# Kernel tuning notes

Hardware: AMD Instinct MI355X
Metric: run time of the kernel (lower is better)

Reference implementation:

```python
import jax, jax.numpy as jnp
from jax import lax
import numpy as np

K = 3          # k_size
STRIDE = 1
LAMDA = 10.0
B, H, W_, D = 2, 64, 64, 64


def extract_patches(x, k, stride, same):
    """TF tf.image.extract_patches layout: per-position vector ordered (ki, kj, channel)."""
    b, h, w, d = x.shape
    kn = (k - 1) // 2
    if same:  # SAME padding, stride 1 (as used for fg patches)
        x = jnp.pad(x, ((0, 0), (kn, kn), (kn, kn), (0, 0)))
        ph, pw = h, w
    else:     # VALID with stride
        ph = (h - k) // stride + 1
        pw = (w - k) // stride + 1
    cols = [x[:, i:i + (ph - 1) * stride + 1:stride, j:j + (pw - 1) * stride + 1:stride, :]
            for i in range(k) for j in range(k)]
    return jnp.stack(cols, axis=3).reshape(b, ph, pw, k * k * d)


def setup_inputs() -> dict:
    key = jax.random.key(0)
    k1, k2, k3, k4 = jax.random.split(key, 4)
    bg_in = jax.random.normal(k1, (B, H, W_, D), jnp.float32)
    fg_in = jax.random.normal(k2, (B, H, W_, D), jnp.float32)
    m = (jax.random.uniform(k3, (B, H, W_, 1)) > 0.3).astype(jnp.float32)
    mask = jnp.broadcast_to(m, (B, H, W_, D)) + jnp.zeros((), jnp.float32)
    W_ml = jax.random.normal(k4, (2 * D, D), jnp.float32) * 0.05  # 1x1 conv 'ML'
    b_ml = jnp.zeros((D,), jnp.float32)
    return {"bg_in": bg_in, "fg_in": fg_in, "mask": mask, "W_ml": W_ml, "b_ml": b_ml}


def reference(bg_in, fg_in, mask, W_ml, b_ml):
    b, h, w, d = bg_in.shape
    kn = (K - 1) // 2
    # nearest resize to (h,w) is identity here; take channel 0, tile to d channels
    mask_r = jnp.broadcast_to(mask[..., :1], (b, h, w, d))
    bg = bg_in * mask_r
    ph = (h - K) // STRIDE + 1
    pw = (w - K) // STRIDE + 1
    c = ph * pw
    # background patches: (b, c, k*k*d); foreground patches: (b, h, w, k*k*d)
    patch1 = extract_patches(bg, K, STRIDE, False).reshape(b, c, K * K * d)
    patch2 = extract_patches(fg_in, K, 1, True)
    k1d = jnp.sum(patch1 * patch1, axis=2)          # (b, c)
    wwd = jnp.sum(patch2 * patch2, axis=3)          # (b, h, w)
    # 1x1 conv of fg patches against bg patch bank == cross-correlation
    CS = jnp.einsum('bhwp,bcp->bhwc', patch2, patch1)
    DS1 = k1d[:, None, None, :] + wwd[..., None] - 2.0 * CS   # squared distances (b,h,w,c)
    mu = jnp.mean(DS1, axis=-1, keepdims=True)
    sd = jnp.std(DS1, axis=-1, keepdims=True)       # population std, as tf.math.reduce_std
    DS2 = -jnp.tanh((DS1 - mu) / sd)
    # exp(x-3)/sum(exp(x-3)) == softmax(x)
    CA = jax.nn.softmax(LAMDA * DS2, axis=-1)       # (b, h, w, c)
    # per-sample transposed conv with bg patches as kernel (k2: (b,K,K,d,c))
    k2 = patch1.reshape(b, c, K, K, d).transpose(0, 2, 3, 4, 1)
    # tf.nn.conv2d_transpose == gradient of SAME conv: correlate with rot180 kernel, swap I/O
    kt = k2[:, ::-1, ::-1].transpose(0, 1, 2, 4, 3)  # (b, K, K, c, d)

    def tconv(ca, ker):
        return lax.conv_general_dilated(ca[None], ker, (1, 1), 'SAME',
                                        dimension_numbers=('NHWC', 'HWIO', 'NHWC'))[0]

    ACL = jax.vmap(tconv)(CA, kt) / float(K * K)    # (b, h, w, d)
    ACL = bg + ACL * (1.0 - mask_r)
    con1 = jnp.concatenate([bg_in, ACL], axis=-1)   # (b, h, w, 2d)
    out = jax.nn.elu(jnp.einsum('bhwc,co->bhwo', con1, W_ml) + b_ml)
    return out
```

## Files before the change

kernel.cpp:

```cpp
#include <hip/hip_runtime.h>
#include <hip/hip_fp16.h>
#include <math.h>

#define BB 2
#define HH 64
#define WW 64
#define DD 64
#define PH 62
#define CC 3844
#define CCP 3968
#define PL 576
#define PLP 640
#define TP 8
#define LAM 10.0f

typedef _Float16 f16;
typedef __attribute__((ext_vector_type(8))) _Float16 half8;
typedef __attribute__((ext_vector_type(4))) float f32x4;

#define REQ_FAST 90030080ULL

__device__ __forceinline__ void gld16(const void* g, void* l) {
  __builtin_amdgcn_global_load_lds((const __attribute__((address_space(1))) void*)g,
                                   (__attribute__((address_space(3))) void*)l, 16, 0, 0);
}

__global__ __launch_bounds__(256) void k_prepA(
    const float* __restrict__ bg_in, const float* __restrict__ fg,
    const float* __restrict__ mask, f16* __restrict__ bgf,
    f16* __restrict__ fgp, float* __restrict__ s2) {
  const int NBG = BB * 4288 * 64;
  const int NFG = BB * 4356 * 64;
  int idx = blockIdx.x * 256 + threadIdx.x;
  if (idx < NBG) {
    int ch = idx & 63;
    int pix = (idx >> 6) % 4288;
    int b = idx / (4288 * 64);
    f16 v = (f16)0.f;
    if (pix < 4096) {
      size_t src = ((size_t)b * 4096 + pix) * 64 + ch;
      v = (f16)(bg_in[src] * mask[((size_t)b * 4096 + pix) * 64]);
    }
    bgf[idx] = v;
  } else if (idx < NBG + NFG) {
    int i2 = idx - NBG;
    int ch = i2 & 63;
    int pix = (i2 >> 6) % 4356;
    int b = i2 / (4356 * 64);
    int yy = pix / 66, xx = pix - 66 * yy;
    float v = 0.f;
    if (yy >= 1 && yy <= 64 && xx >= 1 && xx <= 64)
      v = fg[(((size_t)b * 64 + (yy - 1)) * 64 + (xx - 1)) * 64 + ch];
    fgp[i2] = (f16)v;
  } else {
    int i3 = idx - (NBG + NFG);
    int q = i3 & 15;
    int pix = (i3 >> 4) & 4095;
    int b = i3 >> 16;
    float4 v = ((const float4*)(bg_in + ((size_t)b * 4096 + pix) * 64))[q];
    float a = v.x * v.x + v.y * v.y + v.z * v.z + v.w * v.w;
    a += __shfl_xor(a, 1, 64);
    a += __shfl_xor(a, 2, 64);
    a += __shfl_xor(a, 4, 64);
    a += __shfl_xor(a, 8, 64);
    if (q == 0) {
      float m = mask[((size_t)b * 4096 + pix) * 64];
      s2[b * 4096 + pix] = m * m * a;
    }
  }
}

__global__ __launch_bounds__(256) void k_prepB(
    const f16* __restrict__ bgf, const float* __restrict__ s2,
    f16* __restrict__ P1T, float* __restrict__ k1d) {
  __shared__ f16 st[62 * 66];
  const int NB1 = 31;
  if (blockIdx.x < NB1) {
    int idx = blockIdx.x * 256 + threadIdx.x;
    if (idx < BB * CC) {
      int b = idx / CC, c = idx - b * CC;
      int ci = c / PH, cj = c - ci * PH;
      float s = 0.f;
#pragma unroll
      for (int ki = 0; ki < 3; ++ki)
#pragma unroll
        for (int kj = 0; kj < 3; ++kj)
          s += s2[b * 4096 + (ci + ki) * 64 + cj + kj];
      k1d[(size_t)b * CCP + c] = s;
    }
    return;
  }
  int pb = blockIdx.x - NB1;
  int ci = pb % 63;
  int rest = pb / 63;
  int kk = rest % 9;
  int b = rest / 9;
  int ki = kk / 3, kj = kk - 3 * ki;
  f16* P1Tb = P1T + (size_t)b * PLP * CCP;
  if (ci == 62) {
    for (int i = threadIdx.x; i < 64 * 124; i += 256) {
      int ch = i / 124, cc = i - ch * 124;
      P1Tb[(size_t)(kk * 64 + ch) * CCP + CC + cc] = (f16)0.f;
    }
    return;
  }
  const f16* src = bgf + (size_t)b * (4288 * 64) + (size_t)((ci + ki) * 64 + kj) * 64;
  for (int i = threadIdx.x; i < 496; i += 256) {
    half8 v = ((const half8*)src)[i];
    int p = i >> 3, ch0 = (i & 7) * 8;
#pragma unroll
    for (int j = 0; j < 8; ++j) st[p * 66 + ch0 + j] = v[j];
  }
  __syncthreads();
  for (int i = threadIdx.x; i < 64 * 62; i += 256) {
    int ch = i / 62, cj = i - ch * 62;
    P1Tb[(size_t)(kk * 64 + ch) * CCP + ci * 62 + cj] = st[cj * 66 + ch];
  }
}

__global__ __launch_bounds__(512) void k_gemm1(
    const f16* __restrict__ fgp, const f16* __restrict__ bgf,
    f16* __restrict__ CS) {
  __shared__ f16 tA[2][128 * 64];
  __shared__ f16 tB[2][128 * 64];
  const int tid = threadIdx.x;
  const int l = tid & 63, w = tid >> 6;
  const int b = blockIdx.z;
  const int m0 = blockIdx.y * 128, n0 = blockIdx.x * 128;
  const f16* fgB = fgp + (size_t)b * (4356 * 64);
  const f16* bgB = bgf + (size_t)b * (4288 * 64);

  int pixA[2], chSA[2], aCh[2];
#pragma unroll
  for (int i = 0; i < 2; ++i) {
    aCh[i] = w * 2 + i;
    int li = aCh[i] * 64 + l;
    int r = li >> 3;
    int j = (li & 7) ^ (r & 7);
    chSA[i] = j * 8;
    int pos = m0 + r;
    pixA[i] = (pos >> 6) * 66 + (pos & 63);
  }
  int pixB[2], chSB[2], bCh[2];
#pragma unroll
  for (int i = 0; i < 2; ++i) {
    bCh[i] = w * 2 + i;
    int li = bCh[i] * 64 + l;
    int r = li >> 3;
    int j = (li & 7) ^ (r & 7);
    chSB[i] = j * 8;
    int c = n0 + r;
    if (c < CC) {
      int ci = c / 62;
      pixB[i] = ci * 64 + (c - 62 * ci);
    } else {
      pixB[i] = 4096;
    }
  }

  const int wm = (w >> 2) * 64, wn = (w & 3) * 32;
  const int lr = l & 15, lk = l >> 4;
  const int xr = (lr & 7) << 4;

  f32x4 acc[4][2];
#pragma unroll
  for (int mi = 0; mi < 4; ++mi)
#pragma unroll
    for (int ni = 0; ni < 2; ++ni) acc[mi][ni] = (f32x4){0.f, 0.f, 0.f, 0.f};

#pragma unroll
  for (int i = 0; i < 2; ++i) {
    gld16(fgB + (size_t)pixA[i] * 64 + chSA[i], (char*)tA[0] + aCh[i] * 1024);
    gld16(bgB + (size_t)pixB[i] * 64 + chSB[i], (char*)tB[0] + bCh[i] * 1024);
  }
  asm volatile("s_waitcnt vmcnt(0)" ::: "memory");
  __syncthreads();

#pragma unroll 1
  for (int t = 0; t < 9; ++t) {
    const int cur = t & 1;
    if (t + 1 < 9) {
      const int tn = t + 1;
      const int ki = tn / 3, kj = tn - 3 * ki;
      const int offA = ki * 66 + kj, offB = ki * 64 + kj;
#pragma unroll
      for (int i = 0; i < 2; ++i) {
        gld16(fgB + (size_t)(pixA[i] + offA) * 64 + chSA[i],
              (char*)tA[cur ^ 1] + aCh[i] * 1024);
        gld16(bgB + (size_t)(pixB[i] + offB) * 64 + chSB[i],
              (char*)tB[cur ^ 1] + bCh[i] * 1024);
      }
    }
#pragma unroll
    for (int kk = 0; kk < 2; ++kk) {
      half8 av[4], bv[2];
      const int cb = lk * 16 + kk * 64;
#pragma unroll
      for (int mi = 0; mi < 4; ++mi) {
        int r = wm + mi * 16 + lr;
        av[mi] = *(const half8*)((const char*)tA[cur] + r * 128 + (cb ^ xr));
      }
#pragma unroll
      for (int ni = 0; ni < 2; ++ni) {
        int r = wn + ni * 16 + lr;
        bv[ni] = *(const half8*)((const char*)tB[cur] + r * 128 + (cb ^ xr));
      }
#pragma unroll
      for (int mi = 0; mi < 4; ++mi)
#pragma unroll
        for (int ni = 0; ni < 2; ++ni)
          acc[mi][ni] = __builtin_amdgcn_mfma_f32_16x16x32_f16(
              av[mi], bv[ni], acc[mi][ni], 0, 0, 0);
    }
    asm volatile("s_waitcnt vmcnt(0)" ::: "memory");
    __syncthreads();
  }

  CS += (size_t)b * 4096 * CCP;
#pragma unroll
  for (int mi = 0; mi < 4; ++mi) {
#pragma unroll
    for (int q = 0; q < 4; ++q) {
      int m = m0 + wm + mi * 16 + lk * 4 + q;
#pragma unroll
      for (int ni = 0; ni < 2; ++ni) {
        int n = n0 + wn + ni * 16 + lr;
        CS[(size_t)m * CCP + n] = (f16)acc[mi][ni][q];
      }
    }
  }
}

__global__ __launch_bounds__(512) void k_gemm2(
    const f16* __restrict__ A, const f16* __restrict__ B, f16* __restrict__ C,
    const float* __restrict__ sden) {
  __shared__ f16 tA[2][64 * 64];
  __shared__ f16 tB[2][128 * 64];
  const int tid = threadIdx.x;
  const int l = tid & 63, w = tid >> 6;
  const int p = blockIdx.x;
  const int L = (p & 7) * 80 + (p >> 3);
  const int b = L / 320;
  const int rL = L - b * 320;
  const int mt = rL / 5, nt = rL - mt * 5;
  const int m0 = mt * 64, n0 = nt * 128;
  A += (size_t)b * 4096 * CCP;
  B += (size_t)b * PLP * CCP;
  C += (size_t)b * 4096 * PLP;
  const float* sd = sden + (size_t)b * 4096;

  size_t aOff;
  {
    int li = w * 64 + l;
    int r = li >> 3;
    int j = (li & 7) ^ (r & 7);
    aOff = (size_t)(m0 + r) * CCP + j * 8;
  }
  size_t bOff[2];
  int bCh[2];
#pragma unroll
  for (int i = 0; i < 2; ++i) {
    bCh[i] = w * 2 + i;
    int li = bCh[i] * 64 + l;
    int r = li >> 3;
    int j = (li & 7) ^ (r & 7);
    bOff[i] = (size_t)(n0 + r) * CCP + j * 8;
  }

  const int wm = (w >> 2) * 32, wn = (w & 3) * 32;
  const int lr = l & 15, lk = l >> 4;
  const int xr = (lr & 7) << 4;

  f32x4 acc[2][2];
#pragma unroll
  for (int mi = 0; mi < 2; ++mi)
#pragma unroll
    for (int ni = 0; ni < 2; ++ni) acc[mi][ni] = (f32x4){0.f, 0.f, 0.f, 0.f};

  auto STAGE = [&](int buf, int k0) {
    gld16(A + aOff + k0, (char*)tA[buf] + w * 1024);
#pragma unroll
    for (int i = 0; i < 2; ++i)
      gld16(B + bOff[i] + k0, (char*)tB[buf] + bCh[i] * 1024);
  };

  const int NT = CCP / 64;
  STAGE(0, 0);
  asm volatile("s_waitcnt vmcnt(0)" ::: "memory");
  __syncthreads();

#pragma unroll 1
  for (int t = 0; t < NT; ++t) {
    const int cur = t & 1;
    if (t + 1 < NT) STAGE(cur ^ 1, (t + 1) * 64);
#pragma unroll
    for (int kk = 0; kk < 2; ++kk) {
      half8 av[2], bv[2];
      const int cb = lk * 16 + kk * 64;
#pragma unroll
      for (int mi = 0; mi < 2; ++mi) {
        int r = wm + mi * 16 + lr;
        av[mi] = *(const half8*)((const char*)tA[cur] + r * 128 + (cb ^ xr));
      }
#pragma unroll
      for (int ni = 0; ni < 2; ++ni) {
        int r = wn + ni * 16 + lr;
        bv[ni] = *(const half8*)((const char*)tB[cur] + r * 128 + (cb ^ xr));
      }
#pragma unroll
      for (int mi = 0; mi < 2; ++mi)
#pragma unroll
        for (int ni = 0; ni < 2; ++ni)
          acc[mi][ni] = __builtin_amdgcn_mfma_f32_16x16x32_f16(
              av[mi], bv[ni], acc[mi][ni], 0, 0, 0);
    }
    asm volatile("s_waitcnt vmcnt(0)" ::: "memory");
    __syncthreads();
  }

#pragma unroll
  for (int mi = 0; mi < 2; ++mi) {
#pragma unroll
    for (int q = 0; q < 4; ++q) {
      int m = m0 + wm + mi * 16 + lk * 4 + q;
      float sc = sd[m];
#pragma unroll
      for (int ni = 0; ni < 2; ++ni) {
        int n = n0 + wn + ni * 16 + lr;
        C[(size_t)m * PLP + n] = (f16)(acc[mi][ni][q] * sc);
      }
    }
  }
}

__global__ __launch_bounds__(256) void k_stats(f16* __restrict__ CS,
                                               const float* __restrict__ k1d,
                                               float* __restrict__ sden) {
  __shared__ float red[8];
  const int tid = threadIdx.x;
  const int row = blockIdx.x, b = blockIdx.y;
  f16* cs = CS + ((size_t)b * 4096 + row) * CCP;
  const float* kd = k1d + (size_t)b * CCP;
  const int base = tid * 16;
  const bool act = base < CCP;

  float tv[16];
  float s1 = 0.f, s2 = 0.f;
  if (act) {
    half8 v0 = ((const half8*)(cs + base))[0];
    half8 v1 = ((const half8*)(cs + base))[1];
    float kv[16];
    *(float4*)(kv + 0) = ((const float4*)(kd + base))[0];
    *(float4*)(kv + 4) = ((const float4*)(kd + base))[1];
    *(float4*)(kv + 8) = ((const float4*)(kd + base))[2];
    *(float4*)(kv + 12) = ((const float4*)(kd + base))[3];
#pragma unroll
    for (int i = 0; i < 16; ++i) {
      float cval = (float)(i < 8 ? v0[i] : v1[i - 8]);
      float t = (base + i < CC) ? (kv[i] - 2.f * cval) : 0.f;
      tv[i] = t;
      s1 += t;
      s2 = fmaf(t, t, s2);
    }
  } else {
#pragma unroll
    for (int i = 0; i < 16; ++i) tv[i] = 0.f;
  }
#pragma unroll
  for (int m = 32; m; m >>= 1) {
    s1 += __shfl_xor(s1, m, 64);
    s2 += __shfl_xor(s2, m, 64);
  }
  if ((tid & 63) == 0) {
    red[tid >> 6] = s1;
    red[4 + (tid >> 6)] = s2;
  }
  __syncthreads();
  float mu = (red[0] + red[1] + red[2] + red[3]) * (1.f / CC);
  float ex2 = (red[4] + red[5] + red[6] + red[7]) * (1.f / CC);
  float var = fmaxf(ex2 - mu * mu, 1e-12f);
  float rsd = rsqrtf(var);
  __syncthreads();

  float den = 0.f;
  if (act) {
    half8 w0, w1;
#pragma unroll
    for (int i = 0; i < 16; ++i) {
      float wv = 0.f;
      if (base + i < CC) {
        float z = (tv[i] - mu) * rsd;
        float e2z = __expf(2.f * z);
        float th = 1.f - 2.f / (e2z + 1.f);
        wv = __expf(-LAM * th);
        den += wv;
      }
      if (i < 8) w0[i] = (f16)wv; else w1[i - 8] = (f16)wv;
    }
    ((half8*)(cs + base))[0] = w0;
    ((half8*)(cs + base))[1] = w1;
  }
#pragma unroll
  for (int m = 32; m; m >>= 1) den += __shfl_xor(den, m, 64);
  if ((tid & 63) == 0) red[tid >> 6] = den;
  __syncthreads();
  if (tid == 0)
    sden[(size_t)b * 4096 + row] = 1.f / (9.f * (red[0] + red[1] + red[2] + red[3]));
}

__global__ __launch_bounds__(256) void k_final2(
    const float* __restrict__ bg_in, const float* __restrict__ mask,
    const f16* __restrict__ N2, const float* __restrict__ Wml,
    const float* __restrict__ bml, float* __restrict__ out) {
  __shared__ float s_con[4 * 128];
  const int tid = threadIdx.x;
  const int posg = blockIdx.x * 4;
  for (int i = tid; i < 4 * 128; i += 256) {
    int p = i >> 7, c = i & 127;
    int pos = posg + p;
    float v;
    if (c < 64) {
      v = bg_in[(size_t)pos * DD + c];
    } else {
      int cc = c - 64;
      int bwx = pos & 4095, bb = pos >> 12;
      int y = bwx >> 6, x = bwx & 63;
      float a = 0.f;
#pragma unroll
      for (int s = 0; s < 3; ++s) {
        int yy = y + 1 - s;
        if (yy < 0 || yy >= HH) continue;
#pragma unroll
        for (int t = 0; t < 3; ++t) {
          int xx = x + 1 - t;
          if (xx < 0 || xx >= WW) continue;
          a += (float)N2[((size_t)bb * 4096 + yy * 64 + xx) * PLP + (s * 3 + t) * 64 + cc];
        }
      }
      float m0 = mask[(size_t)pos * DD];
      v = bg_in[(size_t)pos * DD + cc] * m0 + a * (1.f - m0);
    }
    s_con[i] = v;
  }
  __syncthreads();
  const int o = tid & 63, p = tid >> 6;
  float sum = bml[o];
  const float* cp = s_con + (p << 7);
#pragma unroll 8
  for (int c = 0; c < 128; ++c) sum = fmaf(cp[c], Wml[c * 64 + o], sum);
  out[(size_t)(posg + p) * 64 + o] = (sum > 0.f) ? sum : expm1f(sum);
}

#define WS_BG    0
#define WS_BGT   524288
#define WS_K1D   1048576
#define WS_ACLN  1056264

__global__ __launch_bounds__(256) void k_prep(
    const float* __restrict__ bg_in, const float* __restrict__ mask,
    float* __restrict__ bg, float* __restrict__ bgT) {
  int idx = blockIdx.x * 256 + threadIdx.x;
  if (idx >= BB * HH * WW * DD) return;
  int ch = idx & 63, pos = idx >> 6;
  float m = mask[(size_t)pos * DD];
  float v = bg_in[idx] * m;
  bg[idx] = v;
  int x = pos & 63, rest = pos >> 6;
  int y = rest & 63, b = rest >> 6;
  bgT[(((size_t)b * DD + ch) * HH + y) * WW + x] = v;
}

__global__ __launch_bounds__(256) void k_k1d(const float* __restrict__ bg,
                                             float* __restrict__ k1d) {
  int idx = blockIdx.x * 256 + threadIdx.x;
  if (idx >= BB * CC) return;
  int b = idx / CC, c = idx - b * CC;
  int ci = c / PH, cj = c - ci * PH;
  float s = 0.f;
  for (int ki = 0; ki < 3; ++ki)
    for (int kj = 0; kj < 3; ++kj) {
      const float4* p =
          (const float4*)(bg + (((size_t)(b * HH + ci + ki) * WW) + cj + kj) * DD);
#pragma unroll
      for (int q = 0; q < 16; ++q) {
        float4 v = p[q];
        s += v.x * v.x + v.y * v.y + v.z * v.z + v.w * v.w;
      }
    }
  k1d[idx] = s;
}

__global__ __launch_bounds__(256, 2) void k_heavy(
    const float* __restrict__ fg, const float* __restrict__ bg,
    const float* __restrict__ bgT, const float* __restrict__ k1d,
    float* __restrict__ acln) {
  __shared__ _Float16 s_cs[TP * CC];
  __shared__ float s_fg[TP * PL];
  __shared__ float s_red[8];
  __shared__ float s_wwd[TP];
  __shared__ float s_den[TP];

  const int tid = threadIdx.x;
  const int X0 = blockIdx.x * TP;
  const int Y = blockIdx.y;
  const int b = blockIdx.z;

  for (int i = tid; i < TP * PL; i += 256) {
    int p = i / PL, r = i - p * PL;
    int kk = r >> 6, ch = r & 63;
    int ki = kk / 3, kj = kk - 3 * ki;
    int hy = Y + ki - 1, wx = X0 + p + kj - 1;
    float v = 0.f;
    if (hy >= 0 && hy < HH && wx >= 0 && wx < WW)
      v = fg[(((size_t)b * HH + hy) * WW + wx) * DD + ch];
    s_fg[i] = v;
  }
  __syncthreads();
  {
    int p = tid >> 5, lane = tid & 31;
    float a = 0.f;
    for (int r = lane; r < PL; r += 32) {
      float v = s_fg[p * PL + r];
      a = fmaf(v, v, a);
    }
#pragma unroll
    for (int m = 16; m; m >>= 1) a += __shfl_xor(a, m, 64);
    if (lane == 0) s_wwd[p] = a;
  }
  __syncthreads();

  const float* bgTb = bgT + (size_t)b * DD * HH * WW;
  for (int sw = 0; sw < 4; ++sw) {
    const int cb = sw * 256 + tid;
    float acc[TP][4];
#pragma unroll
    for (int p = 0; p < TP; ++p)
#pragma unroll
      for (int q = 0; q < 4; ++q) acc[p][q] = 0.f;
    int off4[4];
#pragma unroll
    for (int q = 0; q < 4; ++q) {
      int c = cb + q * 1024;
      if (c >= CC) c = CC - 1;
      int ci = c / PH;
      off4[q] = ci * WW + (c - ci * PH);
    }
    for (int ch = 0; ch < DD; ++ch) {
      const float* bgTc = bgTb + (size_t)ch * (HH * WW);
#pragma unroll
      for (int kk = 0; kk < 9; ++kk) {
        const int ki = kk / 3, kj = kk - 3 * (kk / 3);
        float fv[TP];
#pragma unroll
        for (int p = 0; p < TP; ++p) fv[p] = s_fg[p * PL + (kk << 6) + ch];
        float bv[4];
#pragma unroll
        for (int q = 0; q < 4; ++q) bv[q] = bgTc[off4[q] + ki * WW + kj];
#pragma unroll
        for (int p = 0; p < TP; ++p)
#pragma unroll
          for (int q = 0; q < 4; ++q) acc[p][q] = fmaf(fv[p], bv[q], acc[p][q]);
      }
    }
#pragma unroll
    for (int q = 0; q < 4; ++q) {
      int c = cb + q * 1024;
      if (c < CC) {
#pragma unroll
        for (int p = 0; p < TP; ++p) s_cs[p * CC + c] = (_Float16)acc[p][q];
      }
    }
  }
  __syncthreads();

  const float* k1db = k1d + b * CC;
  for (int pos = 0; pos < TP; ++pos) {
    __syncthreads();
    const float wwdp = s_wwd[pos];
    float s1 = 0.f, s2 = 0.f;
    for (int c = tid; c < CC; c += 256) {
      float ds1 = k1db[c] + wwdp - 2.f * (float)s_cs[pos * CC + c];
      s1 += ds1;
      s2 = fmaf(ds1, ds1, s2);
    }
#pragma unroll
    for (int m = 32; m; m >>= 1) {
      s1 += __shfl_xor(s1, m, 64);
      s2 += __shfl_xor(s2, m, 64);
    }
    if ((tid & 63) == 0) {
      int w = tid >> 6;
      s_red[w] = s1;
      s_red[4 + w] = s2;
    }
    __syncthreads();
    float mu = (s_red[0] + s_red[1] + s_red[2] + s_red[3]) * (1.f / CC);
    float ex2 = (s_red[4] + s_red[5] + s_red[6] + s_red[7]) * (1.f / CC);
    float var = fmaxf(ex2 - mu * mu, 1e-12f);
    float rsd = rsqrtf(var);
    float dp = 0.f;
    for (int c = tid; c < CC; c += 256) {
      float ds1 = k1db[c] + wwdp - 2.f * (float)s_cs[pos * CC + c];
      float z = (ds1 - mu) * rsd;
      float wv = expf(-LAM * tanhf(z));
      s_cs[pos * CC + c] = (_Float16)wv;
      dp += wv;
    }
#pragma unroll
    for (int m = 32; m; m >>= 1) dp += __shfl_xor(dp, m, 64);
    __syncthreads();
    if ((tid & 63) == 0) s_red[tid >> 6] = dp;
    __syncthreads();
    if (tid == 0) s_den[pos] = s_red[0] + s_red[1] + s_red[2] + s_red[3];
  }

  const int d = tid & 63;
  const int grp = tid >> 6;
  const int oA = grp, oB = grp + 4;
  const int sA = oA / 3, tA = oA - 3 * sA;
  const int sB = oB / 3, tB = oB - 3 * sB;
  const bool hasC = (grp == 0);
  const int offA = (sA * WW + tA) * DD + d;
  const int offB = (sB * WW + tB) * DD + d;
  const int offC = (2 * WW + 2) * DD + d;
  float aA[TP], aB[TP], aC[TP];
#pragma unroll
  for (int p = 0; p < TP; ++p) { aA[p] = 0.f; aB[p] = 0.f; aC[p] = 0.f; }
  const float* bgb = bg + (size_t)b * HH * WW * DD;
  float* s_wf = s_fg;
  int cj = 0, rowoff = 0;
  for (int c0 = 0; c0 < CC; c0 += 128) {
    const int n = (CC - c0 < 128) ? (CC - c0) : 128;
    __syncthreads();
    for (int i = tid; i < TP * 128; i += 256) {
      int p = i >> 7, cc = i & 127;
      s_wf[i] = (cc < n) ? (float)s_cs[p * CC + c0 + cc] : 0.f;
    }
    __syncthreads();
    for (int cc = 0; cc < n; cc += 2) {
      float2 wv[TP];
#pragma unroll
      for (int p = 0; p < TP; ++p)
        wv[p] = *(const float2*)(s_wf + (p << 7) + cc);
      {
        const float* rp = bgb + (size_t)rowoff * DD;
        float bA = rp[offA], bB = rp[offB], bCv = rp[offC];
#pragma unroll
        for (int p = 0; p < TP; ++p) {
          aA[p] = fmaf(wv[p].x, bA, aA[p]);
          aB[p] = fmaf(wv[p].x, bB, aB[p]);
          if (hasC) aC[p] = fmaf(wv[p].x, bCv, aC[p]);
        }
        ++rowoff;
        if (++cj == PH) { cj = 0; rowoff += 2; }
      }
      {
        const float* rp = bgb + (size_t)rowoff * DD;
        float bA = rp[offA], bB = rp[offB], bCv = rp[offC];
#pragma unroll
        for (int p = 0; p < TP; ++p) {
          aA[p] = fmaf(wv[p].y, bA, aA[p]);
          aB[p] = fmaf(wv[p].y, bB, aB[p]);
          if (hasC) aC[p] = fmaf(wv[p].y, bCv, aC[p]);
        }
        ++rowoff;
        if (++cj == PH) { cj = 0; rowoff += 2; }
      }
    }
  }
  __syncthreads();
#pragma unroll
  for (int p = 0; p < TP; ++p) {
    const float inv = 1.f / (9.f * s_den[p]);
    float* dst = acln + ((((size_t)b * HH + Y) * WW + (X0 + p)) * 9) * 64;
    dst[oA * 64 + d] = aA[p] * inv;
    dst[oB * 64 + d] = aB[p] * inv;
    if (hasC) dst[512 + d] = aC[p] * inv;
  }
}

__global__ __launch_bounds__(256) void k_final(
    const float* __restrict__ bg_in, const float* __restrict__ mask,
    const float* __restrict__ bg, const float* __restrict__ acln,
    const float* __restrict__ Wml, const float* __restrict__ bml,
    float* __restrict__ out) {
  __shared__ float s_con[4 * 128];
  const int tid = threadIdx.x;
  const int posg = blockIdx.x * 4;
  for (int i = tid; i < 4 * 128; i += 256) {
    int p = i >> 7, c = i & 127;
    int pos = posg + p;
    float v;
    if (c < 64) {
      v = bg_in[(size_t)pos * DD + c];
    } else {
      int cc = c - 64;
      int bwx = pos & 4095, bb = pos >> 12;
      int y = bwx >> 6, x = bwx & 63;
      float a = 0.f;
#pragma unroll
      for (int s = 0; s < 3; ++s) {
        int yy = y + 1 - s;
        if (yy < 0 || yy >= HH) continue;
#pragma unroll
        for (int t = 0; t < 3; ++t) {
          int xx = x + 1 - t;
          if (xx < 0 || xx >= WW) continue;
          a += acln[((((size_t)bb * HH + yy) * WW + xx) * 9 + (s * 3 + t)) * 64 + cc];
        }
      }
      float m0 = mask[(size_t)pos * DD];
      v = bg[(size_t)pos * DD + cc] + a * (1.f - m0);
    }
    s_con[i] = v;
  }
  __syncthreads();
  const int o = tid & 63, p = tid >> 6;
  float sum = bml[o];
  const float* cp = s_con + (p << 7);
#pragma unroll 8
  for (int c = 0; c < 128; ++c) sum = fmaf(cp[c], Wml[c * 64 + o], sum);
  out[(size_t)(posg + p) * 64 + o] = (sum > 0.f) ? sum : expm1f(sum);
}

extern "C" void kernel_launch(void* const* d_in, const int* in_sizes, int n_in,
                              void* d_out, int out_size, void* d_ws, size_t ws_size,
                              hipStream_t stream) {
  const float* bg_in = (const float*)d_in[0];
  const float* fg_in = (const float*)d_in[1];
  const float* mask = (const float*)d_in[2];
  const float* Wml = (const float*)d_in[3];
  const float* bml = (const float*)d_in[4];
  float* out = (float*)d_out;

  if (ws_size >= REQ_FAST) {
    char* w8 = (char*)d_ws;
    float* s2 = (float*)(w8 + 0);
    f16* fgp = (f16*)(w8 + 2097152);
    f16* bgf = (f16*)(w8 + 3212288);
    f16* P1T = (f16*)(w8 + 4310016);
    f16* CS = (f16*)(w8 + 14468096);
    f16* N2 = (f16*)(w8 + 79479808);
    float* k1d = (float*)(w8 + 89965568);
    float* sden = (float*)(w8 + 89997312);

    const int NA = BB * 4288 * 64 + BB * 4356 * 64 + BB * 4096 * 16;
    k_prepA<<<dim3((NA + 255) / 256), dim3(256), 0, stream>>>(
        bg_in, fg_in, mask, bgf, fgp, s2);
    k_prepB<<<dim3(31 + 63 * 9 * 2), dim3(256), 0, stream>>>(bgf, s2, P1T, k1d);
    k_gemm1<<<dim3(CCP / 128, 32, 2), dim3(512), 0, stream>>>(fgp, bgf, CS);
    k_stats<<<dim3(4096, 2), dim3(256), 0, stream>>>(CS, k1d, sden);
    k_gemm2<<<dim3(640), dim3(512), 0, stream>>>(CS, P1T, N2, sden);
    k_final2<<<dim3(2048), dim3(256), 0, stream>>>(bg_in, mask, N2, Wml, bml, out);
  } else {
    float* ws = (float*)d_ws;
    float* bg = ws + WS_BG;
    float* bgT = ws + WS_BGT;
    float* k1d = ws + WS_K1D;
    float* acln = ws + WS_ACLN;
    k_prep<<<dim3(2048), dim3(256), 0, stream>>>(bg_in, mask, bg, bgT);
    k_k1d<<<dim3((BB * CC + 255) / 256), dim3(256), 0, stream>>>(bg, k1d);
    k_heavy<<<dim3(8, 64, 2), dim3(256), 0, stream>>>(fg_in, bg, bgT, k1d, acln);
    k_final<<<dim3(2048), dim3(256), 0, stream>>>(bg_in, mask, bg, acln, Wml, bml, out);
  }
}
```

Measured before the change: 164.6 us.

## Recompute softmax weights inside gemm2 A-load instead of writing them in stats

k_stats no longer writes the exp/tanh weights back over the CS matrix. It only stores per-row mean, rstd and the normalizer. gemm2 loads the raw CS tile through registers, recomputes the weights on the fly and stores them into LDS, with the B tile still loaded by direct-to-LDS. This drops a full write pass over the large CS buffer. In exchange, the transcendental math is redone in every gemm2 block that shares a row (five column tiles), and the A path moves from async LDS loads to synchronous register loads.

```diff
diff --git a/kernel.cpp b/kernel.cpp
--- a/kernel.cpp
+++ b/kernel.cpp
@@ -231,9 +231,83 @@
   }
 }
 
+__global__ __launch_bounds__(256) void k_stats(const f16* __restrict__ CS,
+                                               const float* __restrict__ k1d,
+                                               float* __restrict__ rstat) {
+  __shared__ float red[8];
+  const int tid = threadIdx.x;
+  const int row = blockIdx.x, b = blockIdx.y;
+  const f16* cs = CS + ((size_t)b * 4096 + row) * CCP;
+  const float* kd = k1d + (size_t)b * CCP;
+  const int base = tid * 16;
+  const bool act = base < CCP;
+
+  float tv[16];
+  float s1 = 0.f, s2 = 0.f;
+  if (act) {
+    half8 v0 = ((const half8*)(cs + base))[0];
+    half8 v1 = ((const half8*)(cs + base))[1];
+    float kv[16];
+    *(float4*)(kv + 0) = ((const float4*)(kd + base))[0];
+    *(float4*)(kv + 4) = ((const float4*)(kd + base))[1];
+    *(float4*)(kv + 8) = ((const float4*)(kd + base))[2];
+    *(float4*)(kv + 12) = ((const float4*)(kd + base))[3];
+#pragma unroll
+    for (int i = 0; i < 16; ++i) {
+      float cval = (float)(i < 8 ? v0[i] : v1[i - 8]);
+      float t = (base + i < CC) ? (kv[i] - 2.f * cval) : 0.f;
+      tv[i] = t;
+      s1 += t;
+      s2 = fmaf(t, t, s2);
+    }
+  } else {
+#pragma unroll
+    for (int i = 0; i < 16; ++i) tv[i] = 0.f;
+  }
+#pragma unroll
+  for (int m = 32; m; m >>= 1) {
+    s1 += __shfl_xor(s1, m, 64);
+    s2 += __shfl_xor(s2, m, 64);
+  }
+  if ((tid & 63) == 0) {
+    red[tid >> 6] = s1;
+    red[4 + (tid >> 6)] = s2;
+  }
+  __syncthreads();
+  float mu = (red[0] + red[1] + red[2] + red[3]) * (1.f / CC);
+  float ex2 = (red[4] + red[5] + red[6] + red[7]) * (1.f / CC);
+  float var = fmaxf(ex2 - mu * mu, 1e-12f);
+  float rsd = rsqrtf(var);
+  __syncthreads();
+
+  float den = 0.f;
+  if (act) {
+#pragma unroll
+    for (int i = 0; i < 16; ++i) {
+      if (base + i < CC) {
+        float z = (tv[i] - mu) * rsd;
+        float e2z = __expf(2.f * z);
+        float th = 1.f - 2.f / (e2z + 1.f);
+        den += __expf(-LAM * th);
+      }
+    }
+  }
+#pragma unroll
+  for (int m = 32; m; m >>= 1) den += __shfl_xor(den, m, 64);
+  if ((tid & 63) == 0) red[tid >> 6] = den;
+  __syncthreads();
+  if (tid == 0) {
+    float dtot = red[0] + red[1] + red[2] + red[3];
+    float* o = rstat + ((size_t)b * 4096 + row) * 4;
+    o[0] = mu;
+    o[1] = rsd;
+    o[2] = 1.f / (9.f * dtot);
+  }
+}
+
 __global__ __launch_bounds__(512) void k_gemm2(
     const f16* __restrict__ A, const f16* __restrict__ B, f16* __restrict__ C,
-    const float* __restrict__ sden) {
+    const float* __restrict__ k1d, const float* __restrict__ rstat) {
   __shared__ f16 tA[2][64 * 64];
   __shared__ f16 tB[2][128 * 64];
   const int tid = threadIdx.x;
@@ -247,23 +321,25 @@
   A += (size_t)b * 4096 * CCP;
   B += (size_t)b * PLP * CCP;
   C += (size_t)b * 4096 * PLP;
-  const float* sd = sden + (size_t)b * 4096;
-
-  size_t aOff;
-  {
-    int li = w * 64 + l;
-    int r = li >> 3;
-    int j = (li & 7) ^ (r & 7);
-    aOff = (size_t)(m0 + r) * CCP + j * 8;
-  }
+  const float* kd = k1d + (size_t)b * CCP;
+  const float* rs = rstat + (size_t)b * 4096 * 4;
+
+  const int li = w * 64 + l;
+  const int aR = li >> 3;
+  const int aJ = (li & 7) ^ (aR & 7);
+  const size_t aOff = (size_t)(m0 + aR) * CCP + aJ * 8;
+  const int aCol0 = aJ * 8;
+  const float muR = rs[(m0 + aR) * 4 + 0];
+  const float rsdR = rs[(m0 + aR) * 4 + 1];
+
   size_t bOff[2];
   int bCh[2];
 #pragma unroll
   for (int i = 0; i < 2; ++i) {
     bCh[i] = w * 2 + i;
-    int li = bCh[i] * 64 + l;
-    int r = li >> 3;
-    int j = (li & 7) ^ (r & 7);
+    int li2 = bCh[i] * 64 + l;
+    int r = li2 >> 3;
+    int j = (li2 & 7) ^ (r & 7);
     bOff[i] = (size_t)(n0 + r) * CCP + j * 8;
   }
 
@@ -277,22 +353,49 @@
 #pragma unroll
     for (int ni = 0; ni < 2; ++ni) acc[mi][ni] = (f32x4){0.f, 0.f, 0.f, 0.f};
 
-  auto STAGE = [&](int buf, int k0) {
-    gld16(A + aOff + k0, (char*)tA[buf] + w * 1024);
-#pragma unroll
-    for (int i = 0; i < 2; ++i)
-      gld16(B + bOff[i] + k0, (char*)tB[buf] + bCh[i] * 1024);
+  auto XF = [&](half8 a8, float4 k0v, float4 k1v, int k0) -> half8 {
+    half8 w8;
+#pragma unroll
+    for (int e = 0; e < 8; ++e) {
+      float kv = (e < 4) ? ((e == 0) ? k0v.x : (e == 1) ? k0v.y : (e == 2) ? k0v.z : k0v.w)
+                         : ((e == 4) ? k1v.x : (e == 5) ? k1v.y : (e == 6) ? k1v.z : k1v.w);
+      float wv = 0.f;
+      if (aCol0 + k0 + e < CC) {
+        float t = kv - 2.f * (float)a8[e];
+        float z = (t - muR) * rsdR;
+        float e2z = __expf(2.f * z);
+        float th = 1.f - 2.f / (e2z + 1.f);
+        wv = __expf(-LAM * th);
+      }
+      w8[e] = (f16)wv;
+    }
+    return w8;
   };
 
   const int NT = CCP / 64;
-  STAGE(0, 0);
-  asm volatile("s_waitcnt vmcnt(0)" ::: "memory");
+  {
+    half8 a8 = *(const half8*)(A + aOff);
+    float4 k0v = *(const float4*)(kd + aCol0);
+    float4 k1v = *(const float4*)(kd + aCol0 + 4);
+    gld16(B + bOff[0], (char*)tB[0] + bCh[0] * 1024);
+    gld16(B + bOff[1], (char*)tB[0] + bCh[1] * 1024);
+    *(half8*)((char*)tA[0] + li * 16) = XF(a8, k0v, k1v, 0);
+  }
   __syncthreads();
 
 #pragma unroll 1
   for (int t = 0; t < NT; ++t) {
     const int cur = t & 1;
-    if (t + 1 < NT) STAGE(cur ^ 1, (t + 1) * 64);
+    half8 a8n;
+    float4 k0n, k1n;
+    if (t + 1 < NT) {
+      const int k0 = (t + 1) * 64;
+      a8n = *(const half8*)(A + aOff + k0);
+      k0n = *(const float4*)(kd + aCol0 + k0);
+      k1n = *(const float4*)(kd + aCol0 + k0 + 4);
+      gld16(B + bOff[0] + k0, (char*)tB[cur ^ 1] + bCh[0] * 1024);
+      gld16(B + bOff[1] + k0, (char*)tB[cur ^ 1] + bCh[1] * 1024);
+    }
 #pragma unroll
     for (int kk = 0; kk < 2; ++kk) {
       half8 av[2], bv[2];
@@ -314,7 +417,8 @@
           acc[mi][ni] = __builtin_amdgcn_mfma_f32_16x16x32_f16(
               av[mi], bv[ni], acc[mi][ni], 0, 0, 0);
     }
-    asm volatile("s_waitcnt vmcnt(0)" ::: "memory");
+    if (t + 1 < NT)
+      *(half8*)((char*)tA[cur ^ 1] + li * 16) = XF(a8n, k0n, k1n, (t + 1) * 64);
     __syncthreads();
   }
 
@@ -323,7 +427,7 @@
 #pragma unroll
     for (int q = 0; q < 4; ++q) {
       int m = m0 + wm + mi * 16 + lk * 4 + q;
-      float sc = sd[m];
+      float sc = rs[m * 4 + 2];
 #pragma unroll
       for (int ni = 0; ni < 2; ++ni) {
         int n = n0 + wn + ni * 16 + lr;
@@ -331,81 +435,6 @@
       }
     }
   }
-}
-
-__global__ __launch_bounds__(256) void k_stats(f16* __restrict__ CS,
-                                               const float* __restrict__ k1d,
-                                               float* __restrict__ sden) {
-  __shared__ float red[8];
-  const int tid = threadIdx.x;
-  const int row = blockIdx.x, b = blockIdx.y;
-  f16* cs = CS + ((size_t)b * 4096 + row) * CCP;
-  const float* kd = k1d + (size_t)b * CCP;
-  const int base = tid * 16;
-  const bool act = base < CCP;
-
-  float tv[16];
-  float s1 = 0.f, s2 = 0.f;
-  if (act) {
-    half8 v0 = ((const half8*)(cs + base))[0];
-    half8 v1 = ((const half8*)(cs + base))[1];
-    float kv[16];
-    *(float4*)(kv + 0) = ((const float4*)(kd + base))[0];
-    *(float4*)(kv + 4) = ((const float4*)(kd + base))[1];
-    *(float4*)(kv + 8) = ((const float4*)(kd + base))[2];
-    *(float4*)(kv + 12) = ((const float4*)(kd + base))[3];
-#pragma unroll
-    for (int i = 0; i < 16; ++i) {
-      float cval = (float)(i < 8 ? v0[i] : v1[i - 8]);
-      float t = (base + i < CC) ? (kv[i] - 2.f * cval) : 0.f;
-      tv[i] = t;
-      s1 += t;
-      s2 = fmaf(t, t, s2);
-    }
-  } else {
-#pragma unroll
-    for (int i = 0; i < 16; ++i) tv[i] = 0.f;
-  }
-#pragma unroll
-  for (int m = 32; m; m >>= 1) {
-    s1 += __shfl_xor(s1, m, 64);
-    s2 += __shfl_xor(s2, m, 64);
-  }
-  if ((tid & 63) == 0) {
-    red[tid >> 6] = s1;
-    red[4 + (tid >> 6)] = s2;
-  }
-  __syncthreads();
-  float mu = (red[0] + red[1] + red[2] + red[3]) * (1.f / CC);
-  float ex2 = (red[4] + red[5] + red[6] + red[7]) * (1.f / CC);
-  float var = fmaxf(ex2 - mu * mu, 1e-12f);
-  float rsd = rsqrtf(var);
-  __syncthreads();
-
-  float den = 0.f;
-  if (act) {
-    half8 w0, w1;
-#pragma unroll
-    for (int i = 0; i < 16; ++i) {
-      float wv = 0.f;
-      if (base + i < CC) {
-        float z = (tv[i] - mu) * rsd;
-        float e2z = __expf(2.f * z);
-        float th = 1.f - 2.f / (e2z + 1.f);
-        wv = __expf(-LAM * th);
-        den += wv;
-      }
-      if (i < 8) w0[i] = (f16)wv; else w1[i - 8] = (f16)wv;
-    }
-    ((half8*)(cs + base))[0] = w0;
-    ((half8*)(cs + base))[1] = w1;
-  }
-#pragma unroll
-  for (int m = 32; m; m >>= 1) den += __shfl_xor(den, m, 64);
-  if ((tid & 63) == 0) red[tid >> 6] = den;
-  __syncthreads();
-  if (tid == 0)
-    sden[(size_t)b * 4096 + row] = 1.f / (9.f * (red[0] + red[1] + red[2] + red[3]));
 }
 
 __global__ __launch_bounds__(256) void k_final2(
@@ -736,21 +765,21 @@
   if (ws_size >= REQ_FAST) {
     char* w8 = (char*)d_ws;
     float* s2 = (float*)(w8 + 0);
+    float* rstat = (float*)(w8 + 524288);
     f16* fgp = (f16*)(w8 + 2097152);
     f16* bgf = (f16*)(w8 + 3212288);
     f16* P1T = (f16*)(w8 + 4310016);
     f16* CS = (f16*)(w8 + 14468096);
     f16* N2 = (f16*)(w8 + 79479808);
     float* k1d = (float*)(w8 + 89965568);
-    float* sden = (float*)(w8 + 89997312);
 
     const int NA = BB * 4288 * 64 + BB * 4356 * 64 + BB * 4096 * 16;
     k_prepA<<<dim3((NA + 255) / 256), dim3(256), 0, stream>>>(
         bg_in, fg_in, mask, bgf, fgp, s2);
     k_prepB<<<dim3(31 + 63 * 9 * 2), dim3(256), 0, stream>>>(bgf, s2, P1T, k1d);
     k_gemm1<<<dim3(CCP / 128, 32, 2), dim3(512), 0, stream>>>(fgp, bgf, CS);
-    k_stats<<<dim3(4096, 2), dim3(256), 0, stream>>>(CS, k1d, sden);
-    k_gemm2<<<dim3(640), dim3(512), 0, stream>>>(CS, P1T, N2, sden);
+    k_stats<<<dim3(4096, 2), dim3(256), 0, stream>>>(CS, k1d, rstat);
+    k_gemm2<<<dim3(640), dim3(512), 0, stream>>>(CS, P1T, N2, k1d, rstat);
     k_final2<<<dim3(2048), dim3(256), 0, stream>>>(bg_in, mask, N2, Wml, bml, out);
   } else {
     float* ws = (float*)d_ws;
```

Result: slower. 274.9 us (+67.0%).
